# Performance work log

Measured on AMD Instinct MI355X. Metric: run time of the kernel, lower is better.

Reference implementation:

```python
import jax, jax.numpy as jnp
import numpy as np

B, CIN, H, W = 8, 4, 64, 64
OUT = 8
K = 3            # kernel side
K2 = K * K       # ReLUKANLayer input_size
G_SIZE = 5       # grid_size
KK = 3           # spline k
G = G_SIZE + KK  # g + k = 8 phases per input element
R = 4.0 * G_SIZE * G_SIZE / ((KK + 1) * (KK + 1))  # 6.25


def setup_inputs() -> dict:
    key = jax.random.key(0)
    k1, k2, k3 = jax.random.split(key, 3)
    x = jax.random.normal(k1, (B, CIN, H, W), dtype=jnp.float32)
    # ReLUKAN phase params: one independent KAN kernel per (out_ch, in_ch)
    pl_base = (jnp.arange(-KK, G_SIZE, dtype=jnp.float32) / G_SIZE)  # (G,)
    phase_low = jnp.broadcast_to(pl_base, (OUT, CIN, K2, G)).astype(jnp.float32)
    phase_high = phase_low + (KK + 1) / G_SIZE
    # equal_size_conv of each ReLUKANLayer: full contraction over (K2, G) -> scalar, plus bias
    weight = jax.random.normal(k2, (OUT, CIN, K2, G), dtype=jnp.float32) / np.sqrt(K2 * G)
    bias = jax.random.normal(k3, (OUT, CIN), dtype=jnp.float32) * 0.01
    return {"x": x, "phase_low": phase_low, "phase_high": phase_high,
            "weight": weight, "bias": bias}


def _patches(x):
    # im2col (torch.nn.Unfold), stride 1, no padding, no dilation
    Bt, C, Ht, Wt = x.shape
    Ho, Wo = Ht - K + 1, Wt - K + 1
    p = jnp.stack([x[:, :, i:i + Ho, j:j + Wo]
                   for i in range(K) for j in range(K)], axis=-1)  # (B,C,Ho,Wo,K2)
    return p.reshape(Bt, C, Ho * Wo, K2), Ho, Wo


def reference(x, phase_low, phase_high, weight, bias):
    # patches: (B, Cin, P, K2)
    patches, Ho, Wo = _patches(x)
    xe = patches[:, None, :, :, :, None]          # (B,1,Cin,P,K2,1)
    pl = phase_low[None, :, :, None, :, :]        # (1,O,Cin,1,K2,G)
    ph = phase_high[None, :, :, None, :, :]
    # ReLUKAN spline basis: (relu(x-pl)*relu(ph-x)*r)^2
    s = (jax.nn.relu(xe - pl) * jax.nn.relu(ph - xe) * R) ** 2  # (B,O,Cin,P,K2,G)
    # full contraction per kernel (equal_size_conv with kernel (G, K2) -> scalar),
    # then accumulate over in-channels per out-channel
    out = jnp.einsum('bocpfg,ocfg->bop', s, weight) + bias.sum(axis=1)[None, :, None]
    return out.reshape(x.shape[0], weight.shape[0], Ho, Wo)
```

## Files before the change

kernel.cpp:

```cpp
#include <hip/hip_runtime.h>

#define B_   8
#define CIN_ 4
#define H_   64
#define W_   64
#define OUT_ 8
#define K_   3
#define K2_  9
#define G_   8
#define HO_  62
#define WO_  62
#define P_   (HO_ * WO_)
#define NPIX (B_ * P_)
#define NBLK ((NPIX + 63) / 64)

__global__ __launch_bounds__(128) void kan_fused(
    const float* __restrict__ x,
    const float* __restrict__ w,
    const float* __restrict__ bias,
    float* __restrict__ out)
{
    const int tid = blockIdx.x * 64 + threadIdx.x;
    const int ob  = threadIdx.y * 4;
    if (tid >= NPIX) return;
    const int b  = tid / P_;
    const int p  = tid - b * P_;
    const int oy = p / WO_;
    const int ox = p - oy * WO_;

    const float RS[G_] = {-2.5f, 0.0f, 2.5f, 5.0f, 7.5f, 10.0f, 12.5f, 15.0f};
    const float RP[G_] = {-0.75f, -1.0f, -0.75f, 0.0f, 1.25f, 3.0f, 5.25f, 8.0f};

    float acc[4];
    #pragma unroll
    for (int oo = 0; oo < 4; ++oo) {
        float s = 0.f;
        #pragma unroll
        for (int c = 0; c < CIN_; ++c) s += bias[(ob + oo) * CIN_ + c];
        acc[oo] = s;
    }

    #pragma unroll 1
    for (int c = 0; c < CIN_; ++c) {
        const float* xc = x + (size_t)(b * CIN_ + c) * (H_ * W_);
        const float* wc = w + (size_t)(ob * CIN_ + c) * (K2_ * G_);
        #pragma unroll
        for (int f = 0; f < K2_; ++f) {
            const int ki = f / 3, kj = f % 3;
            const float xv = xc[(oy + ki) * W_ + ox + kj];
            const float q  = -(6.25f * xv) * xv;
            float mm[G_];
            #pragma unroll
            for (int g = 0; g < G_; ++g) {
                const float t = fmaf(xv, RS[g], q) - RP[g];
                const float m = fmaxf(t, 0.f);
                mm[g] = m * m;
            }
            #pragma unroll
            for (int oo = 0; oo < 4; ++oo) {
                const float* wrow = wc + (size_t)(oo * CIN_) * (K2_ * G_) + f * G_;
                #pragma unroll
                for (int g = 0; g < G_; ++g)
                    acc[oo] = fmaf(mm[g], wrow[g], acc[oo]);
            }
        }
    }

    float* op = out + (size_t)(b * OUT_ + ob) * P_ + p;
    #pragma unroll
    for (int oo = 0; oo < 4; ++oo) op[oo * P_] = acc[oo];
}

extern "C" void kernel_launch(void* const* d_in, const int* in_sizes, int n_in,
                              void* d_out, int out_size, void* d_ws, size_t ws_size,
                              hipStream_t stream) {
    const float* x    = (const float*)d_in[0];
    const float* w    = (const float*)d_in[3];
    const float* bias = (const float*)d_in[4];
    float* out = (float*)d_out;

    kan_fused<<<dim3(NBLK), dim3(64, 2), 0, stream>>>(x, w, bias, out);
}
```

Before: 72.40 us.

## Split input channels across threads and reduce partial sums through LDS

Each input channel is now handled by its own group of threads (block becomes 64x2x4) rather than looped over serially inside one thread. Per-channel partial sums are written to shared memory, and after a barrier each thread adds up the four channels plus the bias for one output channel and pixel. This gives four times as many threads and a shorter serial chain per thread, which should hide latency better. The cost is an extra LDS round trip, a __syncthreads, and 512-thread blocks that may limit register allocation.

```diff
diff --git a/kernel.cpp b/kernel.cpp
--- a/kernel.cpp
+++ b/kernel.cpp
@@ -14,36 +14,32 @@
 #define NPIX (B_ * P_)
 #define NBLK ((NPIX + 63) / 64)
 
-__global__ __launch_bounds__(128) void kan_fused(
+__global__ __launch_bounds__(512) void kan_fused(
     const float* __restrict__ x,
     const float* __restrict__ w,
     const float* __restrict__ bias,
     float* __restrict__ out)
 {
-    const int tid = blockIdx.x * 64 + threadIdx.x;
-    const int ob  = threadIdx.y * 4;
-    if (tid >= NPIX) return;
-    const int b  = tid / P_;
-    const int p  = tid - b * P_;
-    const int oy = p / WO_;
-    const int ox = p - oy * WO_;
+    const int lane  = threadIdx.x;
+    const int ohalf = threadIdx.y;
+    const int c     = threadIdx.z;
+    const int ob    = ohalf * 4;
+    const int tid   = blockIdx.x * 64 + lane;
 
     const float RS[G_] = {-2.5f, 0.0f, 2.5f, 5.0f, 7.5f, 10.0f, 12.5f, 15.0f};
     const float RP[G_] = {-0.75f, -1.0f, -0.75f, 0.0f, 1.25f, 3.0f, 5.25f, 8.0f};
 
-    float acc[4];
-    #pragma unroll
-    for (int oo = 0; oo < 4; ++oo) {
-        float s = 0.f;
-        #pragma unroll
-        for (int c = 0; c < CIN_; ++c) s += bias[(ob + oo) * CIN_ + c];
-        acc[oo] = s;
-    }
+    float acc[4] = {0.f, 0.f, 0.f, 0.f};
 
-    #pragma unroll 1
-    for (int c = 0; c < CIN_; ++c) {
+    if (tid < NPIX) {
+        const int b  = tid / P_;
+        const int p  = tid - b * P_;
+        const int oy = p / WO_;
+        const int ox = p - oy * WO_;
+
         const float* xc = x + (size_t)(b * CIN_ + c) * (H_ * W_);
         const float* wc = w + (size_t)(ob * CIN_ + c) * (K2_ * G_);
+
         #pragma unroll
         for (int f = 0; f < K2_; ++f) {
             const int ki = f / 3, kj = f % 3;
@@ -66,9 +62,25 @@
         }
     }
 
-    float* op = out + (size_t)(b * OUT_ + ob) * P_ + p;
+    __shared__ float lds[CIN_][2][4][64];
     #pragma unroll
-    for (int oo = 0; oo < 4; ++oo) op[oo * P_] = acc[oo];
+    for (int oo = 0; oo < 4; ++oo) lds[c][ohalf][oo][lane] = acc[oo];
+    __syncthreads();
+
+    const int t    = (threadIdx.z * 2 + threadIdx.y) * 64 + threadIdx.x;
+    const int o    = t >> 6;
+    const int pix  = t & 63;
+    const int tid2 = blockIdx.x * 64 + pix;
+    if (tid2 < NPIX) {
+        float s = 0.f;
+        #pragma unroll
+        for (int cc = 0; cc < CIN_; ++cc) s += bias[o * CIN_ + cc];
+        #pragma unroll
+        for (int cc = 0; cc < CIN_; ++cc) s += lds[cc][o >> 2][o & 3][pix];
+        const int b = tid2 / P_;
+        const int p = tid2 - b * P_;
+        out[(size_t)(b * OUT_ + o) * P_ + p] = s;
+    }
 }
 
 extern "C" void kernel_launch(void* const* d_in, const int* in_sizes, int n_in,
@@ -79,5 +91,5 @@
     const float* bias = (const float*)d_in[4];
     float* out = (float*)d_out;
 
-    kan_fused<<<dim3(NBLK), dim3(64, 2), 0, stream>>>(x, w, bias, out);
+    kan_fused<<<dim3(NBLK), dim3(64, 2, 4), 0, stream>>>(x, w, bias, out);
 }
```

After: 70.57 us. -2.5%, faster.
